# Optimization experiments

Hardware: AMD Instinct MI355X
Metric: run time of the kernel (lower is better)

## Reference

```python
import jax, jax.numpy as jnp
import numpy as np

H = 512  # hidden_size == input_size
L = 2    # num_layers
B = 64   # batch
T = 256  # seq_len


def setup_inputs() -> dict:
    key = jax.random.key(0)
    ks = jax.random.split(key, 16)
    def n(k, shape, mean=0.0, std=1.0):
        return mean + std * jax.random.normal(k, shape, dtype=jnp.float32)
    inp = {
        'seq_len': T,
        'init_h': n(ks[0], (L, B, H)),
        'init_c': n(ks[1], (L, B, H)),
        'eps_w': n(ks[2], (T, H, H)),
        'eps_b': n(ks[3], (T, H)),
        # stacked LSTM cell params (PyTorch LSTMCell layout: [4H, in])
        'W_ih0': n(ks[4], (4 * H, H), std=1.0 / np.sqrt(H)),
        'W_hh0': n(ks[5], (4 * H, H), std=1.0 / np.sqrt(H)),
        'b_ih0': n(ks[6], (4 * H,), std=1.0 / np.sqrt(H)),
        'b_hh0': n(ks[7], (4 * H,), std=1.0 / np.sqrt(H)),
        'W_ih1': n(ks[8], (4 * H, H), std=1.0 / np.sqrt(H)),
        'W_hh1': n(ks[9], (4 * H, H), std=1.0 / np.sqrt(H)),
        'b_ih1': n(ks[10], (4 * H,), std=1.0 / np.sqrt(H)),
        'b_hh1': n(ks[11], (4 * H,), std=1.0 / np.sqrt(H)),
        # BayesianLinear params
        'w_mu': n(ks[12], (H, H), std=0.1),
        'w_log_var': n(ks[13], (H, H), mean=-3.0, std=0.1),
        'b_mu': n(ks[14], (H,), std=0.1),
        'b_log_var': n(ks[15], (H,), mean=-3.0, std=0.1),
    }
    return inp


def _lstm_cell(x, h, c, W_ih, W_hh, b_ih, b_hh):
    gates = x @ W_ih.T + b_ih + h @ W_hh.T + b_hh  # [B, 4H]
    i, f, g, o = jnp.split(gates, 4, axis=-1)
    i = jax.nn.sigmoid(i)
    f = jax.nn.sigmoid(f)
    g = jnp.tanh(g)
    o = jax.nn.sigmoid(o)
    c_new = f * c + i * g
    h_new = o * jnp.tanh(c_new)
    return h_new, c_new


def reference(init_h, init_c, eps_w, eps_b,
              W_ih0, W_hh0, b_ih0, b_hh0,
              W_ih1, W_hh1, b_ih1, b_hh1,
              w_mu, w_log_var, b_mu, b_log_var,
              seq_len):
    batch = init_h.shape[1]
    hidden = init_h.shape[2]
    x0 = jnp.zeros((batch, hidden), dtype=init_h.dtype)
    w_sigma = jnp.exp(0.5 * w_log_var)
    b_sigma = jnp.exp(0.5 * b_log_var)

    def step(carry, eps):
        x, h, c = carry  # h,c: [L, B, H]
        ew, eb = eps
        h0, c0 = _lstm_cell(x, h[0], c[0], W_ih0, W_hh0, b_ih0, b_hh0)
        h1, c1 = _lstm_cell(h0, h[1], c[1], W_ih1, W_hh1, b_ih1, b_hh1)
        # BayesianLinear reparameterized sample per step
        w = w_mu + w_sigma * ew
        b = b_mu + b_sigma * eb
        x_next = h1 @ w.T + b
        h_new = jnp.stack([h0, h1])
        c_new = jnp.stack([c0, c1])
        return (x_next, h_new, c_new), h1

    _, out_features = jax.lax.scan(step, (x0, init_h, init_c), (eps_w, eps_b), length=seq_len)
    return out_features  # [seq_len, B, H] (== stacked list of h_last)
```

## Files before the change

### kernel.cpp

```cpp
#include <hip/hip_runtime.h>
#include <hip/hip_bf16.h>

#define T_STEPS 256
#define BATCH   64
#define HID     512
#define NWG     256
#define NTHR    256

typedef float f32x4 __attribute__((ext_vector_type(4)));
typedef short bf16x8 __attribute__((ext_vector_type(8)));
typedef unsigned long long u64;

#define W0OFF   0u
#define W1OFF   65536u
#define WSTOFF  131072u
#define T1OFF   147456u
#define BNCOFF  148480u
#define EBOFF   148992u
#define SMEM_BYTES 149024

__device__ __forceinline__ short f2b(float f) {
  __hip_bfloat16 h = __float2bfloat16(f);
  return *reinterpret_cast<short*>(&h);
}
__device__ __forceinline__ float b2f(short s) {
  __hip_bfloat16 h;
  *reinterpret_cast<short*>(&h) = s;
  return __bfloat162float(h);
}
__device__ __forceinline__ float sigf(float x) { return 1.0f / (1.0f + __expf(-x)); }
__device__ __forceinline__ float tanh_f(float x) { return 2.0f / (1.0f + __expf(-2.0f * x)) - 1.0f; }

__device__ __forceinline__ bf16x8 pack8(float4 a, float4 b) {
  bf16x8 r;
  r[0] = f2b(a.x); r[1] = f2b(a.y); r[2] = f2b(a.z); r[3] = f2b(a.w);
  r[4] = f2b(b.x); r[5] = f2b(b.y); r[6] = f2b(b.z); r[7] = f2b(b.w);
  return r;
}

__device__ __forceinline__ void g_store16(void* p, bf16x8 v) {
  const u64* s = reinterpret_cast<const u64*>(&v);
  u64* d = reinterpret_cast<u64*>(p);
  __hip_atomic_store(d + 0, s[0], __ATOMIC_RELAXED, __HIP_MEMORY_SCOPE_AGENT);
  __hip_atomic_store(d + 1, s[1], __ATOMIC_RELAXED, __HIP_MEMORY_SCOPE_AGENT);
}
__device__ __forceinline__ void llc_load_frag_sync(bf16x8* dst, const unsigned short* p) {
  asm volatile(
      "global_load_dwordx4 %0, %16, off sc0 sc1\n\t"
      "global_load_dwordx4 %1, %16, off offset:64 sc0 sc1\n\t"
      "global_load_dwordx4 %2, %16, off offset:128 sc0 sc1\n\t"
      "global_load_dwordx4 %3, %16, off offset:192 sc0 sc1\n\t"
      "global_load_dwordx4 %4, %16, off offset:256 sc0 sc1\n\t"
      "global_load_dwordx4 %5, %16, off offset:320 sc0 sc1\n\t"
      "global_load_dwordx4 %6, %16, off offset:384 sc0 sc1\n\t"
      "global_load_dwordx4 %7, %16, off offset:448 sc0 sc1\n\t"
      "global_load_dwordx4 %8, %16, off offset:512 sc0 sc1\n\t"
      "global_load_dwordx4 %9, %16, off offset:576 sc0 sc1\n\t"
      "global_load_dwordx4 %10, %16, off offset:640 sc0 sc1\n\t"
      "global_load_dwordx4 %11, %16, off offset:704 sc0 sc1\n\t"
      "global_load_dwordx4 %12, %16, off offset:768 sc0 sc1\n\t"
      "global_load_dwordx4 %13, %16, off offset:832 sc0 sc1\n\t"
      "global_load_dwordx4 %14, %16, off offset:896 sc0 sc1\n\t"
      "global_load_dwordx4 %15, %16, off offset:960 sc0 sc1\n\t"
      "s_waitcnt vmcnt(0)"
      : "=&v"(dst[0]), "=&v"(dst[1]), "=&v"(dst[2]), "=&v"(dst[3]),
        "=&v"(dst[4]), "=&v"(dst[5]), "=&v"(dst[6]), "=&v"(dst[7]),
        "=&v"(dst[8]), "=&v"(dst[9]), "=&v"(dst[10]), "=&v"(dst[11]),
        "=&v"(dst[12]), "=&v"(dst[13]), "=&v"(dst[14]), "=&v"(dst[15])
      : "v"(p)
      : "memory");
}
__device__ __forceinline__ bf16x8 g_load16(const void* p) {
  const u64* s = reinterpret_cast<const u64*>(p);
  union { u64 q[2]; bf16x8 v; } u;
  u.q[0] = __hip_atomic_load(s + 0, __ATOMIC_RELAXED, __HIP_MEMORY_SCOPE_AGENT);
  u.q[1] = __hip_atomic_load(s + 1, __ATOMIC_RELAXED, __HIP_MEMORY_SCOPE_AGENT);
  return u.v;
}
__device__ __forceinline__ void g_load_frag(bf16x8* dst, const unsigned short* p) {
#pragma unroll
  for (int i = 0; i < 16; ++i) dst[i] = g_load16(p + (size_t)i * 32);
}

__device__ __forceinline__ void post_flag(unsigned int* p, unsigned int val) {
  asm volatile("s_waitcnt vmcnt(0)" ::: "memory");
  __hip_atomic_store(p, val, __ATOMIC_RELAXED, __HIP_MEMORY_SCOPE_AGENT);
}
__device__ __forceinline__ void poll_flags(const unsigned int* cohort, unsigned int target) {
  const unsigned int* p = cohort + (threadIdx.x & 63);
  for (;;) {
    unsigned int v = __hip_atomic_load(p, __ATOMIC_RELAXED, __HIP_MEMORY_SCOPE_AGENT);
    if (__all((int)(v >= target))) break;
  }
  __builtin_amdgcn_sched_barrier(0);
}

__device__ __forceinline__ void stage_weights(char* smem, unsigned int base,
                                              const float* Wih, const float* Whh,
                                              int u0, int tid) {
  for (int p = tid; p < 4096; p += NTHR) {
    const int row = p >> 7;
    const int col = (p & 127) * 8;
    const int gate = row >> 3;
    const int grow = gate * 512 + u0 + (row & 7);
    const float* src = (col < 512) ? (Wih + (size_t)grow * HID + col)
                                   : (Whh + (size_t)grow * HID + (col - 512));
    float4 v0 = *(const float4*)src;
    float4 v1 = *(const float4*)(src + 4);
    unsigned int byte = base + (unsigned int)row * 2048u + (unsigned int)col * 2u;
    byte ^= (unsigned int)(row & 7) << 4;
    *(bf16x8*)(smem + byte) = pack8(v0, v1);
  }
}

__device__ __forceinline__ void mm_half(const char* smem, const bf16x8* a, unsigned int wOff,
                                        int brow, int colHalf, int koff, f32x4& A0, f32x4& A1) {
  const unsigned int bb = wOff + (unsigned int)brow * 2048u + (unsigned int)colHalf * 2u;
  const unsigned int sw = (unsigned int)(brow & 7) << 4;
#pragma unroll
  for (int ks = 0; ks < 16; ++ks) {
    bf16x8 b = *(const bf16x8*)(smem + ((bb + (unsigned int)((ks * 32 + koff) * 2)) ^ sw));
    if (ks & 1)
      A1 = __builtin_amdgcn_mfma_f32_16x16x32_bf16(a[ks], b, A1, 0, 0, 0);
    else
      A0 = __builtin_amdgcn_mfma_f32_16x16x32_bf16(a[ks], b, A0, 0, 0, 0);
  }
}

__device__ __forceinline__ void cell_update(char* smem, f32x4 acc, float bt0, float bgb,
                                            float bob, float* cst, float* hv, int lane) {
#pragma unroll
  for (int j = 0; j < 4; ++j) acc[j] += bt0;
  float part[4];
#pragma unroll
  for (int j = 0; j < 4; ++j) part[j] = __shfl_xor(acc[j], 8);
  const float* T1 = (const float*)(smem + T1OFF);
  const int cs = lane & 7;
  const int rb = (lane >> 4) * 4;
#pragma unroll
  for (int j = 0; j < 4; ++j) {
    const float iv = acc[j];
    const float fv = part[j];
    const float gv = T1[(rb + j) * 16 + cs] + bgb;
    const float ov = T1[(rb + j) * 16 + cs + 8] + bob;
    const float cn = sigf(fv) * cst[j] + sigf(iv) * tanh_f(gv);
    cst[j] = cn;
    hv[j] = sigf(ov) * tanh_f(cn);
  }
}

extern "C" __global__ void __launch_bounds__(NTHR, 1)
dlstm_kernel(const float* __restrict__ init_h, const float* __restrict__ init_c,
             const float* __restrict__ eps_w, const float* __restrict__ eps_b,
             const float* __restrict__ W_ih0, const float* __restrict__ W_hh0,
             const float* __restrict__ b_ih0, const float* __restrict__ b_hh0,
             const float* __restrict__ W_ih1, const float* __restrict__ W_hh1,
             const float* __restrict__ b_ih1, const float* __restrict__ b_hh1,
             const float* __restrict__ w_mu, const float* __restrict__ w_log_var,
             const float* __restrict__ b_mu, const float* __restrict__ b_log_var,
             float* __restrict__ out, unsigned int* __restrict__ flags,
             unsigned short* __restrict__ xbuf, unsigned short* __restrict__ h0buf,
             unsigned short* __restrict__ h1buf) {
  extern __shared__ char smem[];
  const int tid = threadIdx.x;
  const int bid = blockIdx.x;
  const int bg = bid & 3;
  const int u  = bid >> 2;
  const int u0 = u * 8;
  const int wave = tid >> 6;
  const int lane = tid & 63;
  const int col = lane & 15;
  const int cs = lane & 7;
  const int rb = (lane >> 4) * 4;
  const int koff = (lane >> 4) * 8;
  const bool is_act = col < 8;
  const size_t BH = (size_t)BATCH * HID;
  unsigned int* cohort = flags + bg * 256;
  unsigned int* myflag = cohort + u;
  const int arow = bg * 16 + col;
  const int brow = wave * 16 + col;

  stage_weights(smem, W0OFF, W_ih0, W_hh0, u0, tid);
  stage_weights(smem, W1OFF, W_ih1, W_hh1, u0, tid);
  {
    bf16x8 z = {0, 0, 0, 0, 0, 0, 0, 0};
    for (int p = tid; p < 512; p += NTHR) {
      const int row = 8 + (p >> 6);
      const int c8 = (p & 63) * 8;
      unsigned int byte = WSTOFF + (unsigned int)row * 1024u + (unsigned int)c8 * 2u;
      byte ^= (unsigned int)(row & 7) << 4;
      *(bf16x8*)(smem + byte) = z;
    }
  }
  float bt0_l0 = 0, bt0_l1 = 0, bgb0 = 0, bob0 = 0, bgb1 = 0, bob1 = 0, bmu_l = 0, bsg_l = 0;
  float c0r[4] = {0, 0, 0, 0}, c1r[4] = {0, 0, 0, 0};
  if (wave == 0) {
    const int ofs = (col < 8) ? 0 : 512;
    const int un = u0 + cs;
    bt0_l0 = b_ih0[ofs + un] + b_hh0[ofs + un];
    bt0_l1 = b_ih1[ofs + un] + b_hh1[ofs + un];
    bgb0 = b_ih0[1024 + un] + b_hh0[1024 + un];
    bob0 = b_ih0[1536 + un] + b_hh0[1536 + un];
    bgb1 = b_ih1[1024 + un] + b_hh1[1024 + un];
    bob1 = b_ih1[1536 + un] + b_hh1[1536 + un];
    bmu_l = b_mu[un];
    bsg_l = __expf(0.5f * b_log_var[un]);
    if (is_act) {
#pragma unroll
      for (int j = 0; j < 4; ++j) {
        c0r[j] = init_c[(size_t)(0 * BATCH + bg * 16 + rb + j) * HID + un];
        c1r[j] = init_c[(size_t)(1 * BATCH + bg * 16 + rb + j) * HID + un];
      }
    }
    if (lane < 16) {
      const int row = bg * 16 + lane;
      const float* s0 = init_h + (size_t)row * HID + u0;
      const float* s1 = init_h + (size_t)(BATCH + row) * HID + u0;
      g_store16(h0buf + (size_t)row * HID + u0,
                pack8(*(const float4*)s0, *(const float4*)(s0 + 4)));
      g_store16(h1buf + (size_t)row * HID + u0,
                pack8(*(const float4*)s1, *(const float4*)(s1 + 4)));
      bf16x8 z = {0, 0, 0, 0, 0, 0, 0, 0};
      g_store16(xbuf + (size_t)row * HID + u0, z);
    }
    if (lane == 0) post_flag(myflag, 1u);
  }
  __syncthreads();

#pragma unroll 1
  for (int t = 0; t < T_STEPS; ++t) {
    const int pp = t & 1;
    const unsigned int tb = 3u * (unsigned int)t;

    bf16x8 sa[16];
    if (wave < 2 && t > 0) {
      g_load_frag(sa, h0buf + (size_t)pp * BH + (size_t)arow * HID + koff);
      __builtin_amdgcn_sched_barrier(0);
    }

    if (wave >= 2) {
      const int q = tid - 128;
      const int erow = q >> 4;
      const int ecb = (q & 15) * 32;
      const float* pm = w_mu + (size_t)(u0 + erow) * HID + ecb;
      const float* pv = w_log_var + (size_t)(u0 + erow) * HID + ecb;
      const float* pe = eps_w + (size_t)t * HID * HID + (size_t)(u0 + erow) * HID + ecb;
      const unsigned int sw = (unsigned int)erow << 4;
      const unsigned int b0 = WSTOFF + (unsigned int)erow * 1024u + (unsigned int)ecb * 2u;
#pragma unroll
      for (int c = 0; c < 4; ++c) {
        bf16x8 v;
#pragma unroll
        for (int qq = 0; qq < 8; ++qq) {
          const int idx = c * 8 + qq;
          v[qq] = f2b(fmaf(__expf(0.5f * pv[idx]), pe[idx], pm[idx]));
        }
        *(bf16x8*)(smem + ((b0 + (unsigned int)c * 16u) ^ sw)) = v;
      }
      if (wave == 3 && lane < 8)
        ((float*)(smem + EBOFF))[lane] = eps_b[(size_t)t * HID + u0 + lane];
    }

    f32x4 g0 = {0.f, 0.f, 0.f, 0.f};
    bf16x8 sth1[16];
    if (wave < 2) {
      poll_flags(cohort, tb + 1u);
      if (t == 0) {
        g_load_frag(sa, h0buf + (size_t)pp * BH + (size_t)arow * HID + koff);
      }
      bf16x8 fa[16];
      llc_load_frag_sync(fa, xbuf + (size_t)pp * BH + (size_t)arow * HID + koff);
      g_load_frag(sth1, h1buf + (size_t)pp * 2 * BH + (size_t)arow * HID + koff);
      __builtin_amdgcn_sched_barrier(0);
      f32x4 A0 = {0, 0, 0, 0}, A1 = {0, 0, 0, 0};
      mm_half(smem, sa, W0OFF, brow, 512, koff, A0, A1);
      mm_half(smem, fa, W0OFF, brow, 0, koff, A0, A1);
      g0 = A0 + A1;
      if (wave == 1) {
        float* T1 = (float*)(smem + T1OFF);
#pragma unroll
        for (int j = 0; j < 4; ++j) T1[(rb + j) * 16 + col] = g0[j];
      }
    }
    __syncthreads();
    if (wave == 0) {
      float hv[4];
      cell_update(smem, g0, bt0_l0, bgb0, bob0, c0r, hv, lane);
      float* BNC = (float*)(smem + BNCOFF);
      if (is_act) {
#pragma unroll
        for (int j = 0; j < 4; ++j) BNC[(rb + j) * 8 + cs] = hv[j];
      }
      asm volatile("s_waitcnt lgkmcnt(0)" ::: "memory");
      if (lane < 16) {
        const int row = bg * 16 + lane;
        float4 v0 = *(float4*)(BNC + lane * 8);
        float4 v1 = *(float4*)(BNC + lane * 8 + 4);
        g_store16(h0buf + (size_t)(pp ^ 1) * BH + (size_t)row * HID + u0, pack8(v0, v1));
      }
      if (lane == 0) post_flag(myflag, tb + 2u);
    }

    f32x4 g1 = {0.f, 0.f, 0.f, 0.f};
    if (wave < 2) {
      poll_flags(cohort, tb + 2u);
      bf16x8 fa[16];
      llc_load_frag_sync(fa, h0buf + (size_t)(pp ^ 1) * BH + (size_t)arow * HID + koff);
      f32x4 A0 = {0, 0, 0, 0}, A1 = {0, 0, 0, 0};
      mm_half(smem, sth1, W1OFF, brow, 512, koff, A0, A1);
      mm_half(smem, fa, W1OFF, brow, 0, koff, A0, A1);
      g1 = A0 + A1;
      if (wave == 1) {
        float* T1 = (float*)(smem + T1OFF);
#pragma unroll
        for (int j = 0; j < 4; ++j) T1[(rb + j) * 16 + col] = g1[j];
      }
    }
    __syncthreads();
    if (wave == 0) {
      float hv[4];
      cell_update(smem, g1, bt0_l1, bgb1, bob1, c1r, hv, lane);
      float* BNC = (float*)(smem + BNCOFF);
      if (is_act) {
#pragma unroll
        for (int j = 0; j < 4; ++j) BNC[(rb + j) * 8 + cs] = hv[j];
      }
      asm volatile("s_waitcnt lgkmcnt(0)" ::: "memory");
      float4 v0 = {0, 0, 0, 0}, v1 = {0, 0, 0, 0};
      if (lane < 16) {
        const int row = bg * 16 + lane;
        v0 = *(float4*)(BNC + lane * 8);
        v1 = *(float4*)(BNC + lane * 8 + 4);
        bf16x8 hi = pack8(v0, v1);
        unsigned short* base = h1buf + (size_t)(pp ^ 1) * 2 * BH;
        g_store16(base + (size_t)row * HID + u0, hi);
        bf16x8 lo;
        const float* va = (const float*)&v0;
        const float* vb = (const float*)&v1;
#pragma unroll
        for (int q = 0; q < 8; ++q) {
          const float f = (q < 4) ? va[q] : vb[q - 4];
          lo[q] = f2b(f - b2f(hi[q]));
        }
        g_store16(base + BH + (size_t)row * HID + u0, lo);
      }
      if (lane == 0) post_flag(myflag, tb + 3u);
      if (lane < 16) {
        const int row = bg * 16 + lane;
        float* od = out + ((size_t)t * BATCH + row) * HID + u0;
        *(float4*)od = v0;
        *(float4*)(od + 4) = v1;
      }
    }

    if (t + 1 < T_STEPS) {
      if (wave == 0) {
        poll_flags(cohort, tb + 3u);
        bf16x8 ahi[16], alo[16];
        const unsigned short* hb =
            h1buf + (size_t)(pp ^ 1) * 2 * BH + (size_t)arow * HID + koff;
        llc_load_frag_sync(ahi, hb);
        llc_load_frag_sync(alo, hb + BH);
        f32x4 A0 = {0, 0, 0, 0}, A1 = {0, 0, 0, 0};
        const unsigned int bb = WSTOFF + (unsigned int)col * 1024u;
        const unsigned int sw = (unsigned int)(col & 7) << 4;
#pragma unroll
        for (int ks = 0; ks < 16; ++ks) {
          bf16x8 b =
              *(const bf16x8*)(smem + ((bb + (unsigned int)((ks * 32 + koff) * 2)) ^ sw));
          A0 = __builtin_amdgcn_mfma_f32_16x16x32_bf16(ahi[ks], b, A0, 0, 0, 0);
          A1 = __builtin_amdgcn_mfma_f32_16x16x32_bf16(alo[ks], b, A1, 0, 0, 0);
        }
        const float ebv = is_act ? ((const float*)(smem + EBOFF))[cs] : 0.f;
        const float xb = bmu_l + bsg_l * ebv;
        f32x4 a2 = A0 + A1;
        float* BNC = (float*)(smem + BNCOFF);
        if (is_act) {
#pragma unroll
          for (int j = 0; j < 4; ++j) BNC[(rb + j) * 8 + cs] = a2[j] + xb;
        }
        asm volatile("s_waitcnt lgkmcnt(0)" ::: "memory");
        if (lane < 16) {
          const int row = bg * 16 + lane;
          float4 v0 = *(float4*)(BNC + lane * 8);
          float4 v1 = *(float4*)(BNC + lane * 8 + 4);
          g_store16(xbuf + (size_t)(pp ^ 1) * BH + (size_t)row * HID + u0, pack8(v0, v1));
        }
        if (lane == 0) post_flag(myflag, tb + 4u);
      }
      __syncthreads();
    }
  }
}

extern "C" void kernel_launch(void* const* d_in, const int* in_sizes, int n_in, void* d_out,
                              int out_size, void* d_ws, size_t ws_size, hipStream_t stream) {
  const float* init_h = (const float*)d_in[1];
  const float* init_c = (const float*)d_in[2];
  const float* eps_w = (const float*)d_in[3];
  const float* eps_b = (const float*)d_in[4];
  const float* W_ih0 = (const float*)d_in[5];
  const float* W_hh0 = (const float*)d_in[6];
  const float* b_ih0 = (const float*)d_in[7];
  const float* b_hh0 = (const float*)d_in[8];
  const float* W_ih1 = (const float*)d_in[9];
  const float* W_hh1 = (const float*)d_in[10];
  const float* b_ih1 = (const float*)d_in[11];
  const float* b_hh1 = (const float*)d_in[12];
  const float* w_mu = (const float*)d_in[13];
  const float* w_log_var = (const float*)d_in[14];
  const float* b_mu = (const float*)d_in[15];
  const float* b_log_var = (const float*)d_in[16];
  float* out = (float*)d_out;

  unsigned char* ws = (unsigned char*)d_ws;
  unsigned int* flags = (unsigned int*)ws;
  unsigned short* xbuf = (unsigned short*)(ws + 131072);
  unsigned short* h0buf = (unsigned short*)(ws + 262144);
  unsigned short* h1buf = (unsigned short*)(ws + 393216);

  hipMemsetAsync(flags, 0, 4 * 256 * sizeof(unsigned int), stream);
  hipFuncSetAttribute((const void*)dlstm_kernel, hipFuncAttributeMaxDynamicSharedMemorySize,
                      SMEM_BYTES);

  void* args[] = {(void*)&init_h, (void*)&init_c, (void*)&eps_w,  (void*)&eps_b,
                  (void*)&W_ih0,  (void*)&W_hh0,  (void*)&b_ih0,  (void*)&b_hh0,
                  (void*)&W_ih1,  (void*)&W_hh1,  (void*)&b_ih1,  (void*)&b_hh1,
                  (void*)&w_mu,   (void*)&w_log_var, (void*)&b_mu, (void*)&b_log_var,
                  (void*)&out,    (void*)&flags,     (void*)&xbuf, (void*)&h0buf,
                  (void*)&h1buf};
  hipError_t err = hipLaunchCooperativeKernel((void*)dlstm_kernel, dim3(NWG), dim3(NTHR), args,
                                              SMEM_BYTES, stream);
  if (err != hipSuccess) {
    hipLaunchKernelGGL(dlstm_kernel, dim3(NWG), dim3(NTHR), SMEM_BYTES, stream, init_h, init_c,
                       eps_w, eps_b, W_ih0, W_hh0, b_ih0, b_hh0, W_ih1, W_hh1, b_ih1, b_hh1,
                       w_mu, w_log_var, b_mu, b_log_var, out, flags, xbuf, h0buf, h1buf);
  }
}
```

Baseline: 5.185 ms.

## Double-buffer sampled Bayesian weights, cache mu/sigma in registers, drop per-step barrier

The sampled BayesianLinear weight tile and eps_b are now double-buffered in LDS by step parity. The per-step __syncthreads at the end of the loop is removed, so the sampling waves can run ahead into the next step. w_mu and exp(0.5*log_var) are loaded once into registers, so each step only reads eps_w with coalesced float4 loads instead of recomputing exp and re-reading mu and log_var. The zero rows used for padding move to a separate region. Without the barrier, correctness now depends on parity buffering and the flag protocol, which risks races if a wave gets two steps ahead.

```diff
diff --git a/kernel.cpp b/kernel.cpp
--- a/kernel.cpp
+++ b/kernel.cpp
@@ -9,15 +9,17 @@
 
 typedef float f32x4 __attribute__((ext_vector_type(4)));
 typedef short bf16x8 __attribute__((ext_vector_type(8)));
+typedef short bf16x4 __attribute__((ext_vector_type(4)));
 typedef unsigned long long u64;
 
 #define W0OFF   0u
 #define W1OFF   65536u
 #define WSTOFF  131072u
-#define T1OFF   147456u
-#define BNCOFF  148480u
-#define EBOFF   148992u
-#define SMEM_BYTES 149024
+#define ZPADOFF 147456u
+#define T1OFF   155648u
+#define BNCOFF  156672u
+#define EBOFF   157184u
+#define SMEM_BYTES 157248
 
 __device__ __forceinline__ short f2b(float f) {
   __hip_bfloat16 h = __float2bfloat16(f);
@@ -184,12 +186,18 @@
   stage_weights(smem, W1OFF, W_ih1, W_hh1, u0, tid);
   {
     bf16x8 z = {0, 0, 0, 0, 0, 0, 0, 0};
-    for (int p = tid; p < 512; p += NTHR) {
-      const int row = 8 + (p >> 6);
-      const int c8 = (p & 63) * 8;
-      unsigned int byte = WSTOFF + (unsigned int)row * 1024u + (unsigned int)c8 * 2u;
-      byte ^= (unsigned int)(row & 7) << 4;
-      *(bf16x8*)(smem + byte) = z;
+    for (int p = tid; p < 512; p += NTHR)
+      *(bf16x8*)(smem + ZPADOFF + (unsigned int)p * 16u) = z;
+  }
+  const int q4 = (tid - 128) * 4;
+  float4 mu4[8], sg4[8];
+  if (wave >= 2) {
+#pragma unroll
+    for (int k = 0; k < 8; ++k) {
+      mu4[k] = *(const float4*)(w_mu + (size_t)(u0 + k) * HID + q4);
+      float4 lv = *(const float4*)(w_log_var + (size_t)(u0 + k) * HID + q4);
+      sg4[k].x = __expf(0.5f * lv.x); sg4[k].y = __expf(0.5f * lv.y);
+      sg4[k].z = __expf(0.5f * lv.z); sg4[k].w = __expf(0.5f * lv.w);
     }
   }
   float bt0_l0 = 0, bt0_l1 = 0, bgb0 = 0, bob0 = 0, bgb1 = 0, bob1 = 0, bmu_l = 0, bsg_l = 0;
@@ -239,26 +247,21 @@
     }
 
     if (wave >= 2) {
-      const int q = tid - 128;
-      const int erow = q >> 4;
-      const int ecb = (q & 15) * 32;
-      const float* pm = w_mu + (size_t)(u0 + erow) * HID + ecb;
-      const float* pv = w_log_var + (size_t)(u0 + erow) * HID + ecb;
-      const float* pe = eps_w + (size_t)t * HID * HID + (size_t)(u0 + erow) * HID + ecb;
-      const unsigned int sw = (unsigned int)erow << 4;
-      const unsigned int b0 = WSTOFF + (unsigned int)erow * 1024u + (unsigned int)ecb * 2u;
-#pragma unroll
-      for (int c = 0; c < 4; ++c) {
-        bf16x8 v;
-#pragma unroll
-        for (int qq = 0; qq < 8; ++qq) {
-          const int idx = c * 8 + qq;
-          v[qq] = f2b(fmaf(__expf(0.5f * pv[idx]), pe[idx], pm[idx]));
-        }
-        *(bf16x8*)(smem + ((b0 + (unsigned int)c * 16u) ^ sw)) = v;
+      const float* pe = eps_w + (size_t)t * HID * HID + (size_t)u0 * HID + q4;
+      const unsigned int wb = WSTOFF + (unsigned int)pp * 8192u + (unsigned int)q4 * 2u;
+#pragma unroll
+      for (int k = 0; k < 8; ++k) {
+        float4 e = *(const float4*)(pe + (size_t)k * HID);
+        bf16x4 v;
+        v[0] = f2b(fmaf(sg4[k].x, e.x, mu4[k].x));
+        v[1] = f2b(fmaf(sg4[k].y, e.y, mu4[k].y));
+        v[2] = f2b(fmaf(sg4[k].z, e.z, mu4[k].z));
+        v[3] = f2b(fmaf(sg4[k].w, e.w, mu4[k].w));
+        unsigned int byte = (wb + (unsigned int)k * 1024u) ^ ((unsigned int)k << 4);
+        *(bf16x4*)(smem + byte) = v;
       }
       if (wave == 3 && lane < 8)
-        ((float*)(smem + EBOFF))[lane] = eps_b[(size_t)t * HID + u0 + lane];
+        ((float*)(smem + EBOFF + pp * 32))[lane] = eps_b[(size_t)t * HID + u0 + lane];
     }
 
     f32x4 g0 = {0.f, 0.f, 0.f, 0.f};
@@ -362,7 +365,9 @@
         llc_load_frag_sync(ahi, hb);
         llc_load_frag_sync(alo, hb + BH);
         f32x4 A0 = {0, 0, 0, 0}, A1 = {0, 0, 0, 0};
-        const unsigned int bb = WSTOFF + (unsigned int)col * 1024u;
+        const unsigned int bb = (col < 8)
+            ? (WSTOFF + (unsigned int)pp * 8192u + (unsigned int)col * 1024u)
+            : (ZPADOFF + (unsigned int)(col - 8) * 1024u);
         const unsigned int sw = (unsigned int)(col & 7) << 4;
 #pragma unroll
         for (int ks = 0; ks < 16; ++ks) {
@@ -371,7 +376,7 @@
           A0 = __builtin_amdgcn_mfma_f32_16x16x32_bf16(ahi[ks], b, A0, 0, 0, 0);
           A1 = __builtin_amdgcn_mfma_f32_16x16x32_bf16(alo[ks], b, A1, 0, 0, 0);
         }
-        const float ebv = is_act ? ((const float*)(smem + EBOFF))[cs] : 0.f;
+        const float ebv = is_act ? ((const float*)(smem + EBOFF + pp * 32))[cs] : 0.f;
         const float xb = bmu_l + bsg_l * ebv;
         f32x4 a2 = A0 + A1;
         float* BNC = (float*)(smem + BNCOFF);
@@ -388,7 +393,6 @@
         }
         if (lane == 0) post_flag(myflag, tb + 4u);
       }
-      __syncthreads();
     }
   }
 }
```

After: 5.107 ms. About the same (-1.5%).
